# Kernel tuning notes

Measured on AMD Instinct MI355X. Metric: run time of the kernel, lower is better.

## Reference

```python
import jax, jax.numpy as jnp
import numpy as np

B, S, D, H = 4, 2048, 1024, 16
DH = D // H
LN_EPS = 1e-5


def setup_inputs() -> dict:
    key = jax.random.key(0)
    ks = jax.random.split(key, 12)
    scale = 0.02
    inp = {
        "x": jax.random.normal(ks[0], (B, S, D), dtype=jnp.float32),
        "attention_mask": jnp.ones((B, 1, 1, S), dtype=jnp.int32),
        # Linear weights stored torch-style: (out_features, in_features)
        "Wq": jax.random.normal(ks[1], (D, D), dtype=jnp.float32) * scale,
        "bq": jax.random.normal(ks[2], (D,), dtype=jnp.float32) * scale,
        "Wk": jax.random.normal(ks[3], (D, D), dtype=jnp.float32) * scale,
        "bk": jax.random.normal(ks[4], (D,), dtype=jnp.float32) * scale,
        "Wv": jax.random.normal(ks[5], (D, D), dtype=jnp.float32) * scale,
        "bv": jax.random.normal(ks[6], (D,), dtype=jnp.float32) * scale,
        "Wo": jax.random.normal(ks[7], (D, D), dtype=jnp.float32) * scale,
        "bo": jax.random.normal(ks[8], (D,), dtype=jnp.float32) * scale,
        "ln_w": jnp.ones((D,), dtype=jnp.float32),
        "ln_b": jnp.zeros((D,), dtype=jnp.float32),
    }
    return inp


def reference(x, attention_mask, Wq, bq, Wk, bk, Wv, bv, Wo, bo, ln_w, ln_b):
    b, s, d = x.shape
    # QKV projections (torch Linear: x @ W.T + b), split into heads -> [b, h, s, dh]
    def proj(W, bias):
        y = jnp.einsum('bsd,ed->bse', x, W) + bias
        return y.reshape(b, s, H, DH).transpose(0, 2, 1, 3)
    q = proj(Wq, bq)
    k = proj(Wk, bk)
    v = proj(Wv, bv)

    scores = jnp.einsum('bhqd,bhkd->bhqk', q, k) / jnp.sqrt(jnp.float32(DH))
    scores = jnp.where(attention_mask == 0, -jnp.inf, scores)
    # max-subtract softmax (stable), identical to jax.nn.softmax
    attn = jax.nn.softmax(scores, axis=-1)
    Hctx = jnp.einsum('bhqk,bhkd->bhqd', attn, v)  # [b, h, s, dh]
    Hctx = Hctx.transpose(0, 2, 1, 3).reshape(b, s, d)

    Hout = jnp.einsum('bsd,ed->bse', Hctx, Wo) + bo
    resid = x + Hout
    mu = jnp.mean(resid, axis=-1, keepdims=True)
    var = jnp.mean(jnp.square(resid - mu), axis=-1, keepdims=True)
    out = (resid - mu) / jnp.sqrt(var + LN_EPS) * ln_w + ln_b
    return out
```

## Files before the change

### kernel.cpp

```cpp
#include <hip/hip_runtime.h>
#include <hip/hip_bf16.h>
#include <stdint.h>

#define Bx  4
#define Sx  2048
#define Dx  1024
#define Hx  16
#define DHx 64
#define Mx  (Bx*Sx)

typedef short bf16x8 __attribute__((ext_vector_type(8)));
typedef float f32x4  __attribute__((ext_vector_type(4)));
typedef float f32x16 __attribute__((ext_vector_type(16)));

#define C1 0.18033688f

__device__ __forceinline__ unsigned short f2bf_u(float f) {
  union { float f; unsigned int u; } c; c.f = f;
  return (unsigned short)((c.u + 0x7fffu + ((c.u >> 16) & 1u)) >> 16);
}
__device__ __forceinline__ unsigned int pack2(float lo, float hi) {
  return ((unsigned int)f2bf_u(hi) << 16) | (unsigned int)f2bf_u(lo);
}
__device__ __forceinline__ unsigned int cvtpk(float lo_, float hi_) {
  unsigned int r;
  asm("v_cvt_pk_bf16_f32 %0, %1, %2" : "=v"(r) : "v"(lo_), "v"(hi_));
  return r;
}
__device__ __forceinline__ void swap32(unsigned int& d, unsigned int& s) {
  asm("v_permlane32_swap_b32 %0, %1" : "+v"(d), "+v"(s));
}

#define GLDS16(gp, lp) __builtin_amdgcn_global_load_lds( \
  (const __attribute__((address_space(1))) unsigned int*)(gp), \
  (__attribute__((address_space(3))) unsigned int*)(lp), 16, 0, 0)

__global__ __launch_bounds__(256) void prep_kernel(
    const float* __restrict__ x,  const float* __restrict__ Wq,
    const float* __restrict__ Wk, const float* __restrict__ Wv,
    const float* __restrict__ Wo, const int* __restrict__ mask,
    uint4* __restrict__ xb4, uint4* __restrict__ wb4,
    float* __restrict__ madd, unsigned* __restrict__ mb) {
  int bid = blockIdx.x, t = threadIdx.x;
  if (bid < 6144) {
    const float* src;
    uint4* dst;
    int i;
    if (bid < 4096) {
      src = x; dst = xb4; i = bid * 256 + t;
    } else {
      int wbid = bid - 4096;
      int widx = wbid >> 9;
      src = (widx == 0) ? Wq : (widx == 1) ? Wk : (widx == 2) ? Wv : Wo;
      dst = wb4 + (size_t)widx * 131072;
      i = (wbid & 511) * 256 + t;
    }
    const float4* s = (const float4*)src + (size_t)i * 2;
    float4 a = s[0], b = s[1];
    uint4 o;
    o.x = pack2(a.x, a.y); o.y = pack2(a.z, a.w);
    o.z = pack2(b.x, b.y); o.w = pack2(b.z, b.w);
    dst[i] = o;
  } else if (bid < 6176) {
    int i = (bid - 6144) * 256 + t;
    madd[i] = (mask[i] == 0) ? -1e30f : 0.0f;
  } else {
    int b = bid - 6176;
    if (t < 64) {
      int any = 0;
      if (t < 32) {
        for (int i = 0; i < 64; ++i) any |= (mask[b * Sx + t * 64 + i] == 0);
      }
      unsigned long long bits = __ballot(any != 0);
      if (t == 0) mb[b] = (unsigned)bits;
    }
  }
}

__global__ __launch_bounds__(256) void qkv_gemm(
    const short* __restrict__ xb, const short* __restrict__ wb,
    const float* __restrict__ bq, const float* __restrict__ bk,
    const float* __restrict__ bv,
    short* __restrict__ qb, short* __restrict__ kb, short* __restrict__ vb) {
  int lid = blockIdx.x + (blockIdx.y << 3) + (blockIdx.z << 9);
  int xcd = lid & 7;
  int idx = lid >> 3;
  int which = idx >> 6;
  int tt = idx & 63;
  int m0 = (xcd * 8 + (tt >> 3)) * 128;
  int n0 = (tt & 7) * 128;

  const short* Wm  = wb + (size_t)which * Dx * Dx;
  const float* bias = (which == 0) ? bq : (which == 1 ? bk : bv);

  __shared__ alignas(16) short smem[128 * 136];
  short* Al = smem;
  short* Bl = smem + 4096;

  int t = threadIdx.x;
  int l = t & 63, w = t >> 6;
  int wm = w >> 1, wn = w & 1;
  int srow = l >> 2;
  int scol = (l & 3) * 8;
  int fr = l & 15, fg = l >> 4;

  f32x4 acc[4][4] = {};

  for (int k0 = 0; k0 < Dx; k0 += 32) {
#pragma unroll
    for (int i = 0; i < 2; ++i) {
      int r0 = (w * 2 + i) * 16;
      const short* ga = xb + (size_t)(m0 + r0 + srow) * Dx + k0 + scol;
      GLDS16(ga, &Al[r0 * 32]);
      const short* gb = Wm + (size_t)(n0 + r0 + srow) * Dx + k0 + scol;
      GLDS16(gb, &Bl[r0 * 32]);
    }
    __syncthreads();
    bf16x8 af[4], bfm[4];
#pragma unroll
    for (int i = 0; i < 4; ++i)
      af[i] = *(const bf16x8*)&Al[(wm * 64 + i * 16 + fr) * 32 + fg * 8];
#pragma unroll
    for (int i = 0; i < 4; ++i)
      bfm[i] = *(const bf16x8*)&Bl[(wn * 64 + i * 16 + fr) * 32 + fg * 8];
#pragma unroll
    for (int mi = 0; mi < 4; ++mi)
#pragma unroll
      for (int ni = 0; ni < 4; ++ni)
        acc[mi][ni] = __builtin_amdgcn_mfma_f32_16x16x32_bf16(
            af[mi], bfm[ni], acc[mi][ni], 0, 0, 0);
    __syncthreads();
  }

  if (which == 2) {
#pragma unroll
    for (int ni = 0; ni < 4; ++ni) {
      int n_l = wn * 64 + ni * 16 + fr;
      float bias_n = bias[n0 + n_l];
#pragma unroll
      for (int mi = 0; mi < 4; ++mi)
#pragma unroll
        for (int r = 0; r < 4; ++r) {
          int m_l = wm * 64 + mi * 16 + fg * 4 + r;
          smem[n_l * 136 + m_l] = (short)f2bf_u(acc[mi][ni][r] + bias_n);
        }
    }
    __syncthreads();
    int b = m0 >> 11, s0_ = m0 & 2047;
#pragma unroll
    for (int it = 0; it < 8; ++it) {
      int idx2 = t + it * 256;
      int n_l = idx2 >> 4, c = idx2 & 15;
      int4 v = *(const int4*)&smem[n_l * 136 + c * 8];
      int n = n0 + n_l, h = n >> 6, dh = n & 63;
      int chunk = (c & 7) ^ (dh & 7);
      size_t off = (size_t)(b * Hx + h) * Sx * 64
                 + (size_t)((s0_ >> 6) + (c >> 3)) * 4096
                 + dh * 64 + chunk * 8;
      *(int4*)&vb[off] = v;
    }
    return;
  }

#pragma unroll
  for (int ni = 0; ni < 4; ++ni) {
    int n = n0 + wn * 64 + ni * 16 + fr;
    int h = n >> 6, dh = n & 63;
    float bias_n = bias[n];
#pragma unroll
    for (int mi = 0; mi < 4; ++mi) {
#pragma unroll
      for (int r = 0; r < 4; ++r) {
        int m = m0 + wm * 64 + mi * 16 + fg * 4 + r;
        int b = m >> 11, s = m & 2047;
        float y = acc[mi][ni][r] + bias_n;
        size_t hb = (size_t)(b * Hx + h) * Sx * DHx;
        if (which == 0) {
          qb[hb + (size_t)s * DHx + dh] = (short)f2bf_u(y * C1);
        } else {
          kb[hb + (size_t)s * 64 + ((((dh >> 3) ^ (s & 7)) << 3) | (dh & 7))] =
              (short)f2bf_u(y);
        }
      }
    }
  }
}

__global__ __launch_bounds__(256) void attn_kernel(
    const short* __restrict__ qb, const short* __restrict__ kb,
    const short* __restrict__ vb, const float* __restrict__ madd,
    const unsigned* __restrict__ maskbits, short* __restrict__ cbuf) {
  int bh = blockIdx.x;
  int qt = blockIdx.y;
  int b  = bh >> 4;

  __shared__ alignas(16) short Kl[2][4096];
  __shared__ alignas(16) short Vt[2][4096];

  int t = threadIdx.x, l = t & 63, w = t >> 6;
  int lo = l & 31, hi = l >> 5;

  const short* qg = qb + ((size_t)bh * Sx + qt * 128 + w * 32 + lo) * 64;
  bf16x8 qf[4];
#pragma unroll
  for (int ks = 0; ks < 4; ++ks)
    qf[ks] = *(const bf16x8*)&qg[ks * 16 + hi * 8];

  const short* kg = kb + (size_t)bh * Sx * 64;
  const short* vg = vb + (size_t)bh * Sx * 64;
  const float* mg = madd + b * Sx;
  unsigned mbits = maskbits[b];

  bf16x8 ones;
#pragma unroll
  for (int i = 0; i < 8; ++i) ones[i] = (short)0x3F80;

  f32x16 O0 = {}, O1 = {}, Ssum = {};

#define STAGE(tile, bf) do {                                              \
    const short* ks_ = kg + (size_t)(tile) * 4096;                        \
    const short* vs_ = vg + (size_t)(tile) * 4096;                        \
    GLDS16(ks_ + w * 512 + l * 8,        &Kl[bf][w * 512]);               \
    GLDS16(ks_ + 2048 + w * 512 + l * 8, &Kl[bf][2048 + w * 512]);        \
    GLDS16(vs_ + w * 512 + l * 8,        &Vt[bf][w * 512]);               \
    GLDS16(vs_ + 2048 + w * 512 + l * 8, &Vt[bf][2048 + w * 512]);        \
  } while (0)

  STAGE(0, 0);

  for (int tile = 0; tile < 32; ++tile) {
    int cur = tile & 1;
    if (tile < 31) {
      STAGE(tile + 1, cur ^ 1);
      asm volatile("s_waitcnt vmcnt(4)" ::: "memory");
    } else {
      asm volatile("s_waitcnt vmcnt(0)" ::: "memory");
    }
    __builtin_amdgcn_s_barrier();

    const short* Kb = &Kl[cur][0];
    const short* Vb = &Vt[cur][0];

    f32x16 st0 = {}, st1 = {};
    __builtin_amdgcn_s_setprio(1);
#pragma unroll
    for (int ks = 0; ks < 4; ++ks) {
      bf16x8 kf = *(const bf16x8*)&Kb[lo * 64 + (((2 * ks + hi) ^ (lo & 7)) << 3)];
      st0 = __builtin_amdgcn_mfma_f32_32x32x16_bf16(kf, qf[ks], st0, 0, 0, 0);
    }
#pragma unroll
    for (int ks = 0; ks < 4; ++ks) {
      bf16x8 kf = *(const bf16x8*)&Kb[(32 + lo) * 64 + (((2 * ks + hi) ^ (lo & 7)) << 3)];
      st1 = __builtin_amdgcn_mfma_f32_32x32x16_bf16(kf, qf[ks], st1, 0, 0, 0);
    }
    __builtin_amdgcn_s_setprio(0);

    if ((mbits >> tile) & 1) {
      const float* mrow = mg + tile * 64;
#pragma unroll
      for (int r = 0; r < 16; ++r) {
        int key = (r & 3) + 8 * (r >> 2) + 4 * hi;
        st0[r] += mrow[key];
        st1[r] += mrow[32 + key];
      }
    }

#pragma unroll
    for (int r = 0; r < 16; ++r) {
      st0[r] = __builtin_amdgcn_exp2f(st0[r]);
      st1[r] = __builtin_amdgcn_exp2f(st1[r]);
    }

    __builtin_amdgcn_s_setprio(1);
#pragma unroll
    for (int kbi = 0; kbi < 2; ++kbi) {
#pragma unroll
      for (int half = 0; half < 2; ++half) {
        int po = half * 8;
        unsigned int u, u2, v, v2;
        if (kbi == 0) {
          u  = cvtpk(st0[po + 0], st0[po + 1]);
          u2 = cvtpk(st0[po + 2], st0[po + 3]);
          v  = cvtpk(st0[po + 4], st0[po + 5]);
          v2 = cvtpk(st0[po + 6], st0[po + 7]);
        } else {
          u  = cvtpk(st1[po + 0], st1[po + 1]);
          u2 = cvtpk(st1[po + 2], st1[po + 3]);
          v  = cvtpk(st1[po + 4], st1[po + 5]);
          v2 = cvtpk(st1[po + 6], st1[po + 7]);
        }
        swap32(v, u);
        swap32(v2, u2);
        union { unsigned int i[4]; bf16x8 v8; } pu;
        pu.i[0] = u; pu.i[1] = u2; pu.i[2] = v; pu.i[3] = v2;
        int tt = kbi * 2 + half;
        bf16x8 vf0 = *(const bf16x8*)&Vb[lo * 64 + (((2 * tt + hi) ^ (lo & 7)) << 3)];
        bf16x8 vf1 = *(const bf16x8*)&Vb[(32 + lo) * 64 + (((2 * tt + hi) ^ (lo & 7)) << 3)];
        O0 = __builtin_amdgcn_mfma_f32_32x32x16_bf16(pu.v8, vf0, O0, 0, 0, 0);
        O1 = __builtin_amdgcn_mfma_f32_32x32x16_bf16(pu.v8, vf1, O1, 0, 0, 0);
        Ssum = __builtin_amdgcn_mfma_f32_32x32x16_bf16(pu.v8, ones, Ssum, 0, 0, 0);
      }
    }
    __builtin_amdgcn_s_setprio(0);

    __builtin_amdgcn_s_barrier();
  }
#undef STAGE

  int h = bh & 15, bq_ = bh >> 4;
#pragma unroll
  for (int a = 0; a < 4; ++a) {
#pragma unroll
    for (int j = 0; j < 4; ++j) {
      int r = a * 4 + j;
      float linv = __builtin_amdgcn_rcpf(Ssum[r]);
      int s = qt * 128 + w * 32 + a * 8 + hi * 4 + j;
      size_t rowb = ((size_t)(bq_ * Sx + s)) * Dx + h * 64;
      cbuf[rowb + lo]      = (short)f2bf_u(O0[r] * linv);
      cbuf[rowb + 32 + lo] = (short)f2bf_u(O1[r] * linv);
    }
  }
}

__global__ __launch_bounds__(256) void proj_gemm(
    const short* __restrict__ cb, const short* __restrict__ wo,
    const float* __restrict__ bo, const float* __restrict__ x,
    float* __restrict__ out) {
  int lid = blockIdx.x + (blockIdx.y << 3);
  int xcd = lid & 7;
  int tt = lid >> 3;
  int m0 = (xcd * 8 + (tt >> 3)) * 128;
  int n0 = (tt & 7) * 128;

  __shared__ alignas(16) short Al[128 * 32];
  __shared__ alignas(16) short Bl[128 * 32];

  int t = threadIdx.x;
  int l = t & 63, w = t >> 6;
  int wm = w >> 1, wn = w & 1;
  int srow = l >> 2, scol = (l & 3) * 8;
  int fr = l & 15, fg = l >> 4;

  f32x4 acc[4][4] = {};

  for (int k0 = 0; k0 < Dx; k0 += 32) {
#pragma unroll
    for (int i = 0; i < 2; ++i) {
      int r0 = (w * 2 + i) * 16;
      const short* ga = cb + (size_t)(m0 + r0 + srow) * Dx + k0 + scol;
      GLDS16(ga, &Al[r0 * 32]);
      const short* gb = wo + (size_t)(n0 + r0 + srow) * Dx + k0 + scol;
      GLDS16(gb, &Bl[r0 * 32]);
    }
    __syncthreads();
    bf16x8 af[4], bfm[4];
#pragma unroll
    for (int i = 0; i < 4; ++i)
      af[i] = *(const bf16x8*)&Al[(wm * 64 + i * 16 + fr) * 32 + fg * 8];
#pragma unroll
    for (int i = 0; i < 4; ++i)
      bfm[i] = *(const bf16x8*)&Bl[(wn * 64 + i * 16 + fr) * 32 + fg * 8];
#pragma unroll
    for (int mi = 0; mi < 4; ++mi)
#pragma unroll
      for (int ni = 0; ni < 4; ++ni)
        acc[mi][ni] = __builtin_amdgcn_mfma_f32_16x16x32_bf16(
            af[mi], bfm[ni], acc[mi][ni], 0, 0, 0);
    __syncthreads();
  }

#pragma unroll
  for (int ni = 0; ni < 4; ++ni) {
    int n = n0 + wn * 64 + ni * 16 + fr;
    float bias_n = bo[n];
#pragma unroll
    for (int mi = 0; mi < 4; ++mi) {
#pragma unroll
      for (int r = 0; r < 4; ++r) {
        int m = m0 + wm * 64 + mi * 16 + fg * 4 + r;
        float y = acc[mi][ni][r] + bias_n + x[(size_t)m * Dx + n];
        out[(size_t)m * Dx + n] = y;
      }
    }
  }
}

__global__ __launch_bounds__(256) void ln_kernel(float* __restrict__ io,
                                                 const float* __restrict__ lw,
                                                 const float* __restrict__ lb) {
  int row = blockIdx.x;
  float* p = io + (size_t)row * Dx;
  int c = threadIdx.x * 4;
  float4 v = *(float4*)&p[c];
  float s = v.x + v.y + v.z + v.w;
  float q = v.x * v.x + v.y * v.y + v.z * v.z + v.w * v.w;
#pragma unroll
  for (int d = 1; d < 64; d <<= 1) {
    s += __shfl_xor(s, d, 64);
    q += __shfl_xor(q, d, 64);
  }
  __shared__ float ss[4], qq[4];
  int l = threadIdx.x & 63, w = threadIdx.x >> 6;
  if (l == 0) { ss[w] = s; qq[w] = q; }
  __syncthreads();
  s = ss[0] + ss[1] + ss[2] + ss[3];
  q = qq[0] + qq[1] + qq[2] + qq[3];
  float mu = s * (1.f / Dx);
  float var = q * (1.f / Dx) - mu * mu;
  float rstd = rsqrtf(var + 1e-5f);
  float4 w4 = *(const float4*)&lw[c];
  float4 b4 = *(const float4*)&lb[c];
  float4 o;
  o.x = (v.x - mu) * rstd * w4.x + b4.x;
  o.y = (v.y - mu) * rstd * w4.y + b4.y;
  o.z = (v.z - mu) * rstd * w4.z + b4.z;
  o.w = (v.w - mu) * rstd * w4.w + b4.w;
  *(float4*)&p[c] = o;
}

extern "C" void kernel_launch(void* const* d_in, const int* in_sizes, int n_in,
                              void* d_out, int out_size, void* d_ws, size_t ws_size,
                              hipStream_t stream) {
  const float* x   = (const float*)d_in[0];
  const int*   msk = (const int*)d_in[1];
  const float* Wq  = (const float*)d_in[2];
  const float* bq  = (const float*)d_in[3];
  const float* Wk  = (const float*)d_in[4];
  const float* bk  = (const float*)d_in[5];
  const float* Wv  = (const float*)d_in[6];
  const float* bv  = (const float*)d_in[7];
  const float* Wo  = (const float*)d_in[8];
  const float* bo  = (const float*)d_in[9];
  const float* lnw = (const float*)d_in[10];
  const float* lnb = (const float*)d_in[11];
  float* out = (float*)d_out;

  char* ws = (char*)d_ws;
  short* xb = (short*)(ws);
  short* wb = (short*)(ws + (size_t)(16 << 20));
  short* qb = (short*)(ws + (size_t)(24 << 20));
  short* kb = (short*)(ws + (size_t)(40 << 20));
  short* vb = (short*)(ws + (size_t)(56 << 20));
  short* cb = (short*)(ws + (size_t)(72 << 20));
  float* madd = out;
  unsigned* mbits = (unsigned*)(out + Mx);

  prep_kernel<<<6180, 256, 0, stream>>>(x, Wq, Wk, Wv, Wo, msk,
                                        (uint4*)xb, (uint4*)wb, madd, mbits);
  qkv_gemm<<<dim3(8, 64, 3), 256, 0, stream>>>(xb, wb, bq, bk, bv, qb, kb, vb);
  attn_kernel<<<dim3(64, 16), 256, 0, stream>>>(qb, kb, vb, madd, mbits, cb);
  proj_gemm<<<dim3(8, 64), 256, 0, stream>>>(cb, wb + 3 * (size_t)(Dx * Dx), bo, x, out);
  ln_kernel<<<Mx, 256, 0, stream>>>(out, lnw, lnb);
}
```

Measured before the change: 222.8 us.

## Double-buffer LDS tiles in QKV and output projection GEMMs

Both the QKV and output-projection GEMMs now use two LDS stages: the global-to-LDS loads for the next K step are issued before computing on the current buffer. A partial vmcnt wait and raw s_barrier replace the full __syncthreads, and MFMA sections are bracketed with s_setprio to favour math issue. This aims to hide global load latency behind MFMA work, at the cost of doubling LDS use in proj_gemm and depending on hand-tuned waitcnt correctness.

```diff
diff --git a/kernel.cpp b/kernel.cpp
--- a/kernel.cpp
+++ b/kernel.cpp
@@ -94,8 +94,6 @@
   const float* bias = (which == 0) ? bq : (which == 1 ? bk : bv);
 
   __shared__ alignas(16) short smem[128 * 136];
-  short* Al = smem;
-  short* Bl = smem + 4096;
 
   int t = threadIdx.x;
   int l = t & 63, w = t >> 6;
@@ -106,16 +104,32 @@
 
   f32x4 acc[4][4] = {};
 
-  for (int k0 = 0; k0 < Dx; k0 += 32) {
-#pragma unroll
-    for (int i = 0; i < 2; ++i) {
-      int r0 = (w * 2 + i) * 16;
-      const short* ga = xb + (size_t)(m0 + r0 + srow) * Dx + k0 + scol;
-      GLDS16(ga, &Al[r0 * 32]);
-      const short* gb = Wm + (size_t)(n0 + r0 + srow) * Dx + k0 + scol;
-      GLDS16(gb, &Bl[r0 * 32]);
-    }
-    __syncthreads();
+#define QSTAGE(step, bf) do {                                                  \
+    int kk = (step) * 32;                                                      \
+    _Pragma("unroll")                                                          \
+    for (int i = 0; i < 2; ++i) {                                              \
+      int r0 = (w * 2 + i) * 16;                                               \
+      GLDS16(xb + (size_t)(m0 + r0 + srow) * Dx + kk + scol,                   \
+             &smem[(bf) * 8192 + r0 * 32]);                                    \
+      GLDS16(Wm + (size_t)(n0 + r0 + srow) * Dx + kk + scol,                   \
+             &smem[(bf) * 8192 + 4096 + r0 * 32]);                             \
+    }                                                                          \
+  } while (0)
+
+  QSTAGE(0, 0);
+
+  for (int ks = 0; ks < 32; ++ks) {
+    int cur = ks & 1;
+    if (ks < 31) {
+      QSTAGE(ks + 1, cur ^ 1);
+      asm volatile("s_waitcnt vmcnt(4)" ::: "memory");
+    } else {
+      asm volatile("s_waitcnt vmcnt(0)" ::: "memory");
+    }
+    __builtin_amdgcn_s_barrier();
+
+    const short* Al = &smem[cur * 8192];
+    const short* Bl = &smem[cur * 8192 + 4096];
     bf16x8 af[4], bfm[4];
 #pragma unroll
     for (int i = 0; i < 4; ++i)
@@ -123,14 +137,17 @@
 #pragma unroll
     for (int i = 0; i < 4; ++i)
       bfm[i] = *(const bf16x8*)&Bl[(wn * 64 + i * 16 + fr) * 32 + fg * 8];
+    __builtin_amdgcn_s_setprio(1);
 #pragma unroll
     for (int mi = 0; mi < 4; ++mi)
 #pragma unroll
       for (int ni = 0; ni < 4; ++ni)
         acc[mi][ni] = __builtin_amdgcn_mfma_f32_16x16x32_bf16(
             af[mi], bfm[ni], acc[mi][ni], 0, 0, 0);
-    __syncthreads();
-  }
+    __builtin_amdgcn_s_setprio(0);
+    __builtin_amdgcn_s_barrier();
+  }
+#undef QSTAGE
 
   if (which == 2) {
 #pragma unroll
@@ -332,8 +349,7 @@
   int m0 = (xcd * 8 + (tt >> 3)) * 128;
   int n0 = (tt & 7) * 128;
 
-  __shared__ alignas(16) short Al[128 * 32];
-  __shared__ alignas(16) short Bl[128 * 32];
+  __shared__ alignas(16) short smem[2 * 8192];
 
   int t = threadIdx.x;
   int l = t & 63, w = t >> 6;
@@ -343,16 +359,32 @@
 
   f32x4 acc[4][4] = {};
 
-  for (int k0 = 0; k0 < Dx; k0 += 32) {
-#pragma unroll
-    for (int i = 0; i < 2; ++i) {
-      int r0 = (w * 2 + i) * 16;
-      const short* ga = cb + (size_t)(m0 + r0 + srow) * Dx + k0 + scol;
-      GLDS16(ga, &Al[r0 * 32]);
-      const short* gb = wo + (size_t)(n0 + r0 + srow) * Dx + k0 + scol;
-      GLDS16(gb, &Bl[r0 * 32]);
-    }
-    __syncthreads();
+#define PSTAGE(step, bf) do {                                                  \
+    int kk = (step) * 32;                                                      \
+    _Pragma("unroll")                                                          \
+    for (int i = 0; i < 2; ++i) {                                              \
+      int r0 = (w * 2 + i) * 16;                                               \
+      GLDS16(cb + (size_t)(m0 + r0 + srow) * Dx + kk + scol,                   \
+             &smem[(bf) * 8192 + r0 * 32]);                                    \
+      GLDS16(wo + (size_t)(n0 + r0 + srow) * Dx + kk + scol,                   \
+             &smem[(bf) * 8192 + 4096 + r0 * 32]);                             \
+    }                                                                          \
+  } while (0)
+
+  PSTAGE(0, 0);
+
+  for (int ks = 0; ks < 32; ++ks) {
+    int cur = ks & 1;
+    if (ks < 31) {
+      PSTAGE(ks + 1, cur ^ 1);
+      asm volatile("s_waitcnt vmcnt(4)" ::: "memory");
+    } else {
+      asm volatile("s_waitcnt vmcnt(0)" ::: "memory");
+    }
+    __builtin_amdgcn_s_barrier();
+
+    const short* Al = &smem[cur * 8192];
+    const short* Bl = &smem[cur * 8192 + 4096];
     bf16x8 af[4], bfm[4];
 #pragma unroll
     for (int i = 0; i < 4; ++i)
@@ -360,14 +392,17 @@
 #pragma unroll
     for (int i = 0; i < 4; ++i)
       bfm[i] = *(const bf16x8*)&Bl[(wn * 64 + i * 16 + fr) * 32 + fg * 8];
+    __builtin_amdgcn_s_setprio(1);
 #pragma unroll
     for (int mi = 0; mi < 4; ++mi)
 #pragma unroll
       for (int ni = 0; ni < 4; ++ni)
         acc[mi][ni] = __builtin_amdgcn_mfma_f32_16x16x32_bf16(
             af[mi], bfm[ni], acc[mi][ni], 0, 0, 0);
-    __syncthreads();
-  }
+    __builtin_amdgcn_s_setprio(0);
+    __builtin_amdgcn_s_barrier();
+  }
+#undef PSTAGE
 
 #pragma unroll
   for (int ni = 0; ni < 4; ++ni) {
```

New measurement: 230.7 us. 3.5% more time.
